# Performance work log

Measured on AMD Instinct MI355X. Metric: run time of the kernel, lower is better.

The kernel has to match this reference:

```python
import jax, jax.numpy as jnp
import numpy as np

B, N_SRC, N_DST, E, F = 2, 131072, 131072, 524288, 64
EPS = 1e-8


def setup_inputs() -> dict:
    key = jax.random.key(0)
    k1, k2, k3 = jax.random.split(key, 3)
    x = jax.random.normal(k1, (B, N_SRC, F), dtype=jnp.float32)
    edge_index = jax.random.randint(k2, (2, E), 0, N_DST, dtype=jnp.int64)
    weights = jax.random.uniform(k3, (E,), dtype=jnp.float32)
    return {"x": x, "edge_index": edge_index, "weights": weights}


def reference(x, edge_index, weights):
    src = edge_index[0]  # (E,) indices into source nodes
    dst = edge_index[1]  # (E,) indices into destination nodes
    # _row_normalize_weights: normalize per destination node
    norm = jax.ops.segment_sum(weights, dst, num_segments=N_DST)  # (N_DST,)
    w = weights / (norm[dst] + EPS)  # (E,)
    # Batched SpMM: out[b, d, :] = sum_{e: dst[e]==d} w[e] * x[b, src[e], :]
    gathered = x[:, src, :] * w[None, :, None]  # (B, E, F)
    out = jnp.zeros((B, N_DST, F), dtype=x.dtype).at[:, dst, :].add(gathered)
    return out
```

## Files before the change

### kernel.cpp

```cpp
#include <hip/hip_runtime.h>

#define NB    2
#define NDST  131072
#define NSRC  131072
#define FF    64
#define EE    524288
#define EPSV  1e-8f

#define NBUCK  2048
#define NSEG   2
#define SEGCAP 224
#define CAPB   (NSEG * SEGCAP)
#define CPAD   32
#define NCUR   (NBUCK * NSEG)

typedef unsigned long long u64;

__global__ void init_kernel(int4* __restrict__ gcur4) {
    gcur4[blockIdx.x * 256 + threadIdx.x] = int4{0, 0, 0, 0};
}

__global__ __launch_bounds__(256) void scatter_kernel(const int* __restrict__ src,
                                                      const int* __restrict__ dst,
                                                      const float* __restrict__ wts,
                                                      int* __restrict__ gcur,
                                                      u64* __restrict__ rec) {
    int t   = threadIdx.x;
    int blk = blockIdx.x;
    int seg = blk & (NSEG - 1);
    int base = blk * 1024 + t;
    int d[4]; int s[4]; float w[4];
    #pragma unroll
    for (int i = 0; i < 4; ++i) {
        int e = base + i * 256;
        d[i] = dst[e]; s[i] = src[e]; w[i] = wts[e];
    }
    #pragma unroll
    for (int i = 0; i < 4; ++i) {
        int b    = d[i] >> 6;
        int cell = b * NSEG + seg;
        int p    = atomicAdd(&gcur[cell << 5], 1);
        u64 r = ((u64)__float_as_uint(w[i]) << 32)
              | ((u64)(d[i] & 63) << 17)
              | (unsigned)s[i];
        if (p < SEGCAP) rec[(size_t)cell * SEGCAP + p] = r;
    }
}

__global__ __launch_bounds__(256) void fused_kernel(const float* __restrict__ x,
                                                    const int* __restrict__ gcur,
                                                    const u64* __restrict__ rec,
                                                    float* __restrict__ out) {
    __shared__ u64 stage[CAPB];
    __shared__ u64 sorted[CAPB];
    __shared__ int cnt[64];
    __shared__ int loffs[65];

    int t = threadIdx.x;
    int k = blockIdx.x;
    int n0 = gcur[(k * NSEG + 0) << 5]; if (n0 > SEGCAP) n0 = SEGCAP;
    int n1 = gcur[(k * NSEG + 1) << 5]; if (n1 > SEGCAP) n1 = SEGCAP;
    const u64* __restrict__ b0 = rec + (size_t)(k * NSEG + 0) * SEGCAP;
    const u64* __restrict__ b1 = rec + (size_t)(k * NSEG + 1) * SEGCAP;
    int n = n0 + n1;

    if (t < 64) cnt[t] = 0;
    __syncthreads();

    for (int i = t; i < n0; i += 256) {
        u64 r = b0[i];
        stage[i] = r;
        atomicAdd(&cnt[(int)((r >> 17) & 63)], 1);
    }
    for (int i = t; i < n1; i += 256) {
        u64 r = b1[i];
        stage[n0 + i] = r;
        atomicAdd(&cnt[(int)((r >> 17) & 63)], 1);
    }
    __syncthreads();

    if (t < 64) {
        int c = cnt[t];
        int incl = c;
        #pragma unroll
        for (int off = 1; off < 64; off <<= 1) {
            int o = __shfl_up(incl, off, 64);
            if (t >= off) incl += o;
        }
        loffs[t + 1] = incl;
        if (t == 0) loffs[0] = 0;
        cnt[t] = incl - c;
    }
    __syncthreads();

    for (int i = t; i < n; i += 256) {
        u64 r = stage[i];
        int p = atomicAdd(&cnt[(int)((r >> 17) & 63)], 1);
        sorted[p] = r;
    }
    __syncthreads();

    int wave = t >> 6, lane = t & 63;
    const float* xb0 = x + lane;
    const float* xb1 = x + (size_t)NSRC * FF + lane;

    for (int dl = wave * 16; dl < wave * 16 + 16; ++dl) {
        int begin = loffs[dl];
        int end   = loffs[dl + 1];
        float acc0 = 0.f, acc1 = 0.f, sumw = 0.f;
        int e = begin;
        for (; e + 4 <= end; e += 4) {
            u64 r0 = sorted[e + 0];
            u64 r1 = sorted[e + 1];
            u64 r2 = sorted[e + 2];
            u64 r3 = sorted[e + 3];
            int s0 = (int)(r0 & 0x1FFFF);  float w0 = __uint_as_float((unsigned)(r0 >> 32));
            int s1 = (int)(r1 & 0x1FFFF);  float w1 = __uint_as_float((unsigned)(r1 >> 32));
            int s2 = (int)(r2 & 0x1FFFF);  float w2 = __uint_as_float((unsigned)(r2 >> 32));
            int s3 = (int)(r3 & 0x1FFFF);  float w3 = __uint_as_float((unsigned)(r3 >> 32));
            float a00 = xb0[(size_t)s0 * FF];
            float a10 = xb0[(size_t)s1 * FF];
            float a20 = xb0[(size_t)s2 * FF];
            float a30 = xb0[(size_t)s3 * FF];
            float a01 = xb1[(size_t)s0 * FF];
            float a11 = xb1[(size_t)s1 * FF];
            float a21 = xb1[(size_t)s2 * FF];
            float a31 = xb1[(size_t)s3 * FF];
            sumw += (w0 + w1) + (w2 + w3);
            acc0 = fmaf(w0, a00, fmaf(w1, a10, fmaf(w2, a20, fmaf(w3, a30, acc0))));
            acc1 = fmaf(w0, a01, fmaf(w1, a11, fmaf(w2, a21, fmaf(w3, a31, acc1))));
        }
        for (; e < end; ++e) {
            u64 r = sorted[e];
            int s = (int)(r & 0x1FFFF);
            float w = __uint_as_float((unsigned)(r >> 32));
            sumw += w;
            acc0 = fmaf(w, xb0[(size_t)s * FF], acc0);
            acc1 = fmaf(w, xb1[(size_t)s * FF], acc1);
        }
        float inv = 1.0f / (sumw + EPSV);
        int d = k * 64 + dl;
        __builtin_nontemporal_store(acc0 * inv, &out[(size_t)d * FF + lane]);
        __builtin_nontemporal_store(acc1 * inv, &out[(size_t)NDST * FF + (size_t)d * FF + lane]);
    }
}

extern "C" void kernel_launch(void* const* d_in, const int* in_sizes, int n_in,
                              void* d_out, int out_size, void* d_ws, size_t ws_size,
                              hipStream_t stream) {
    const float* x          = (const float*)d_in[0];
    const int*   edge_index = (const int*)d_in[1];
    const float* weights    = (const float*)d_in[2];

    const int* src = edge_index;
    const int* dst = edge_index + EE;
    float* out = (float*)d_out;

    int* gcur = (int*)d_ws;
    u64* rec  = (u64*)((char*)d_ws + (size_t)NCUR * CPAD * sizeof(int));

    init_kernel<<<(NCUR * CPAD / 4) / 256, 256, 0, stream>>>((int4*)gcur);
    scatter_kernel<<<EE / 1024, 256, 0, stream>>>(src, dst, weights, gcur, rec);
    fused_kernel<<<NBUCK, 256, 0, stream>>>(x, gcur, rec, out);
}
```

Measured before the change: 170.5 us.

## Flatten per-wave edge loop with 8-wide gathers and batch scatter atomics

```diff
diff --git a/kernel.cpp b/kernel.cpp
--- a/kernel.cpp
+++ b/kernel.cpp
@@ -28,22 +28,29 @@
     int t   = threadIdx.x;
     int blk = blockIdx.x;
     int seg = blk & (NSEG - 1);
-    int base = blk * 1024 + t;
-    int d[4]; int s[4]; float w[4];
+    int base = blk * 2048 + t;
+    int d[8]; int s[8]; float w[8];
     #pragma unroll
-    for (int i = 0; i < 4; ++i) {
+    for (int i = 0; i < 8; ++i) {
         int e = base + i * 256;
-        d[i] = dst[e]; s[i] = src[e]; w[i] = wts[e];
+        d[i] = __builtin_nontemporal_load(&dst[e]);
+        s[i] = __builtin_nontemporal_load(&src[e]);
+        w[i] = __builtin_nontemporal_load(&wts[e]);
+    }
+    int p[8];
+    #pragma unroll
+    for (int i = 0; i < 8; ++i) {
+        int cell = (d[i] >> 6) * NSEG + seg;
+        p[i] = atomicAdd(&gcur[cell << 5], 1);
     }
     #pragma unroll
-    for (int i = 0; i < 4; ++i) {
-        int b    = d[i] >> 6;
-        int cell = b * NSEG + seg;
-        int p    = atomicAdd(&gcur[cell << 5], 1);
+    for (int i = 0; i < 8; ++i) {
+        int cell = (d[i] >> 6) * NSEG + seg;
         u64 r = ((u64)__float_as_uint(w[i]) << 32)
               | ((u64)(d[i] & 63) << 17)
               | (unsigned)s[i];
-        if (p < SEGCAP) rec[(size_t)cell * SEGCAP + p] = r;
+        if (p[i] < SEGCAP)
+            __builtin_nontemporal_store(r, &rec[(size_t)cell * SEGCAP + p[i]]);
     }
 }
 
@@ -68,12 +75,12 @@
     __syncthreads();
 
     for (int i = t; i < n0; i += 256) {
-        u64 r = b0[i];
+        u64 r = __builtin_nontemporal_load(&b0[i]);
         stage[i] = r;
         atomicAdd(&cnt[(int)((r >> 17) & 63)], 1);
     }
     for (int i = t; i < n1; i += 256) {
-        u64 r = b1[i];
+        u64 r = __builtin_nontemporal_load(&b1[i]);
         stage[n0 + i] = r;
         atomicAdd(&cnt[(int)((r >> 17) & 63)], 1);
     }
@@ -101,47 +108,55 @@
     __syncthreads();
 
     int wave = t >> 6, lane = t & 63;
+    int dlo = wave * 16, dhi = dlo + 16;
+    int begin = loffs[dlo];
+    int end   = loffs[dhi];
     const float* xb0 = x + lane;
     const float* xb1 = x + (size_t)NSRC * FF + lane;
+    float* ob0 = out + lane + (size_t)(k * 64) * FF;
+    float* ob1 = ob0 + (size_t)NDST * FF;
 
-    for (int dl = wave * 16; dl < wave * 16 + 16; ++dl) {
-        int begin = loffs[dl];
-        int end   = loffs[dl + 1];
-        float acc0 = 0.f, acc1 = 0.f, sumw = 0.f;
-        int e = begin;
-        for (; e + 4 <= end; e += 4) {
-            u64 r0 = sorted[e + 0];
-            u64 r1 = sorted[e + 1];
-            u64 r2 = sorted[e + 2];
-            u64 r3 = sorted[e + 3];
-            int s0 = (int)(r0 & 0x1FFFF);  float w0 = __uint_as_float((unsigned)(r0 >> 32));
-            int s1 = (int)(r1 & 0x1FFFF);  float w1 = __uint_as_float((unsigned)(r1 >> 32));
-            int s2 = (int)(r2 & 0x1FFFF);  float w2 = __uint_as_float((unsigned)(r2 >> 32));
-            int s3 = (int)(r3 & 0x1FFFF);  float w3 = __uint_as_float((unsigned)(r3 >> 32));
-            float a00 = xb0[(size_t)s0 * FF];
-            float a10 = xb0[(size_t)s1 * FF];
-            float a20 = xb0[(size_t)s2 * FF];
-            float a30 = xb0[(size_t)s3 * FF];
-            float a01 = xb1[(size_t)s0 * FF];
-            float a11 = xb1[(size_t)s1 * FF];
-            float a21 = xb1[(size_t)s2 * FF];
-            float a31 = xb1[(size_t)s3 * FF];
-            sumw += (w0 + w1) + (w2 + w3);
-            acc0 = fmaf(w0, a00, fmaf(w1, a10, fmaf(w2, a20, fmaf(w3, a30, acc0))));
-            acc1 = fmaf(w0, a01, fmaf(w1, a11, fmaf(w2, a21, fmaf(w3, a31, acc1))));
+    float acc0 = 0.f, acc1 = 0.f, sumw = 0.f;
+    int cur = dlo;
+
+    for (int i = begin; i < end; i += 8) {
+        int rem = end - i;
+        u64 r[8];
+        #pragma unroll
+        for (int j = 0; j < 8; ++j)
+            r[j] = (j < rem) ? sorted[i + j] : 0ULL;
+
+        float a0[8], a1[8], w[8]; int bn[8];
+        #pragma unroll
+        for (int j = 0; j < 8; ++j) {
+            int s  = (int)(r[j] & 0x1FFFF);
+            w[j]   = __uint_as_float((unsigned)(r[j] >> 32));
+            bn[j]  = (int)((r[j] >> 17) & 63);
+            a0[j]  = xb0[(size_t)s * FF];
+            a1[j]  = xb1[(size_t)s * FF];
         }
-        for (; e < end; ++e) {
-            u64 r = sorted[e];
-            int s = (int)(r & 0x1FFFF);
-            float w = __uint_as_float((unsigned)(r >> 32));
-            sumw += w;
-            acc0 = fmaf(w, xb0[(size_t)s * FF], acc0);
-            acc1 = fmaf(w, xb1[(size_t)s * FF], acc1);
+        #pragma unroll
+        for (int j = 0; j < 8; ++j) {
+            if (bn[j] > cur) {
+                do {
+                    float inv = 1.0f / (sumw + EPSV);
+                    __builtin_nontemporal_store(acc0 * inv, &ob0[(size_t)cur * FF]);
+                    __builtin_nontemporal_store(acc1 * inv, &ob1[(size_t)cur * FF]);
+                    acc0 = 0.f; acc1 = 0.f; sumw = 0.f;
+                    ++cur;
+                } while (cur < bn[j]);
+            }
+            sumw += w[j];
+            acc0 = fmaf(w[j], a0[j], acc0);
+            acc1 = fmaf(w[j], a1[j], acc1);
         }
+    }
+    while (cur < dhi) {
         float inv = 1.0f / (sumw + EPSV);
-        int d = k * 64 + dl;
-        __builtin_nontemporal_store(acc0 * inv, &out[(size_t)d * FF + lane]);
-        __builtin_nontemporal_store(acc1 * inv, &out[(size_t)NDST * FF + (size_t)d * FF + lane]);
+        __builtin_nontemporal_store(acc0 * inv, &ob0[(size_t)cur * FF]);
+        __builtin_nontemporal_store(acc1 * inv, &ob1[(size_t)cur * FF]);
+        acc0 = 0.f; acc1 = 0.f; sumw = 0.f;
+        ++cur;
     }
 }
 
@@ -160,6 +175,6 @@
     u64* rec  = (u64*)((char*)d_ws + (size_t)NCUR * CPAD * sizeof(int));
 
     init_kernel<<<(NCUR * CPAD / 4) / 256, 256, 0, stream>>>((int4*)gcur);
-    scatter_kernel<<<EE / 1024, 256, 0, stream>>>(src, dst, weights, gcur, rec);
+    scatter_kernel<<<EE / 2048, 256, 0, stream>>>(src, dst, weights, gcur, rec);
     fused_kernel<<<NBUCK, 256, 0, stream>>>(x, gcur, rec, out);
 }
```

New measurement: 177.9 us. 4.4% more time.
